# Kernel tuning notes

Measured on AMD Instinct MI355X. Metric: run time of the kernel, lower is better.

The kernel has to match this reference:

```python
import math
import jax, jax.numpy as jnp
import numpy as np

D_MODEL, D_K, D_V = 512, 64, 64
B, S = 4, 4096

def setup_inputs() -> dict:
    key = jax.random.key(0)
    ks = jax.random.split(key, 7)
    scale_in = 1.0 / math.sqrt(D_MODEL)
    return {
        "x": jax.random.normal(ks[0], (B, S, D_MODEL), dtype=jnp.float32),
        "wq": jax.random.normal(ks[1], (D_MODEL, D_K), dtype=jnp.float32) * scale_in,
        "bq": jax.random.normal(ks[2], (D_K,), dtype=jnp.float32) * 0.02,
        "wk": jax.random.normal(ks[3], (D_MODEL, D_K), dtype=jnp.float32) * scale_in,
        "bk": jax.random.normal(ks[4], (D_K,), dtype=jnp.float32) * 0.02,
        "wv": jax.random.normal(ks[5], (D_MODEL, D_V), dtype=jnp.float32) * scale_in,
        "bv": jax.random.normal(ks[6], (D_V,), dtype=jnp.float32) * 0.02,
    }

def reference(x, wq, bq, wk, bk, wv, bv):
    # q,k: [B,S,Dk]; v: [B,S,Dv]
    q = jnp.einsum("bsd,dk->bsk", x, wq) + bq
    k = jnp.einsum("bsd,dk->bsk", x, wk) + bk
    v = jnp.einsum("bsd,dv->bsv", x, wv) + bv
    inv_sqrt_dk = 1.0 / math.sqrt(D_K)
    scores = jnp.einsum("bqk,bsk->bqs", q, k) * inv_sqrt_dk  # [B,S,S]
    probs = jax.nn.softmax(scores, axis=2)
    return jnp.einsum("bqs,bsv->bqv", probs, v)  # [B,S,Dv]
```

## Files before the change

kernel.cpp:

```cpp
#include <hip/hip_runtime.h>
#include <hip/hip_bf16.h>
#include <cstddef>
#include <cstdint>

#define DM 512
#define DK 64
#define BB 4
#define S4 4096
#define NR (BB*S4)
#define KVB 64
#define QBLOCK 128
#define LP 72

typedef float   f32x16 __attribute__((ext_vector_type(16)));
typedef short   bf16x8 __attribute__((ext_vector_type(8)));

#define QSCALE 0.18033688011112042f

__device__ __forceinline__ ushort bf16bits(float f) {
    __hip_bfloat16 h = __float2bfloat16(f);
    return *reinterpret_cast<ushort*>(&h);
}

__device__ __forceinline__ uint32_t cvtpk(float a, float b) {
    uint32_t d;
    asm("v_cvt_pk_bf16_f32 %0, %1, %2" : "=v"(d) : "v"(a), "v"(b));
    return d;
}

__device__ __forceinline__ void permswap(uint32_t& a, uint32_t& b) {
    asm("v_permlane32_swap_b32 %0, %1" : "+v"(a), "+v"(b));
}

__global__ __launch_bounds__(256) void prep_w(
    const float* __restrict__ wq, const float* __restrict__ wk,
    const float* __restrict__ wv,
    ushort* __restrict__ Wfh, ushort* __restrict__ Wfl)
{
    const int id = blockIdx.x * 256 + threadIdx.x;
    const int c  = id >> 9, k = id & 511;
    const float* src = (c < 64) ? wq : (c < 128) ? wk : wv;
    const float wval = src[k * DK + (c & 63)];
    const ushort h  = bf16bits(wval);
    __hip_bfloat16 hh = *reinterpret_cast<const __hip_bfloat16*>(&h);
    const ushort l  = bf16bits(wval - __bfloat162float(hh));
    const int ko = k >> 6, ks = (k >> 4) & 3, kh = (k >> 3) & 1, e = k & 7;
    const size_t idx = ((size_t)((ko * 4 + ks) * 2 + kh) * 192 + c) * 8 + e;
    Wfh[idx] = h;
    Wfl[idx] = l;
}

__global__ __launch_bounds__(256, 3) void qkv_mfma(
    const float* __restrict__ x,
    const ushort* __restrict__ Wfh, const ushort* __restrict__ Wfl,
    const float* __restrict__ bq, const float* __restrict__ bk,
    const float* __restrict__ bv,
    ushort* __restrict__ Qb, ushort* __restrict__ Kb, ushort* __restrict__ Vt)
{
    __shared__ ushort Xw[4][2][32 * 72];

    const int tid  = threadIdx.x;
    const int w    = tid >> 6;
    const int lane = tid & 63;
    const int hi   = lane >> 5;
    const int q5   = lane & 31;
    const int wr   = w >> 1, wc = w & 1;
    const size_t row0 = (size_t)blockIdx.x * 64;
    const int cidx = blockIdx.y * 2 + wc;
    const int lrow = lane >> 4;
    const int lcol = lane & 15;

    float4 xr[8];
    uint2  cw[8];

    auto gx = [&](int ko) {
        #pragma unroll
        for (int i = 0; i < 8; ++i) {
            const int r = wr * 32 + i * 4 + lrow;
            xr[i] = *(const float4*)&x[(row0 + r) * DM + ko * 64 + lcol * 4];
        }
    };
    auto cvt_all = [&]() {
        #pragma unroll
        for (int i = 0; i < 8; ++i)
            cw[i] = (uint2){cvtpk(xr[i].x, xr[i].y), cvtpk(xr[i].z, xr[i].w)};
    };
    auto wstage = [&](int buf) {
        ushort* base = &Xw[w][buf][0];
        #pragma unroll
        for (int i = 0; i < 8; ++i) {
            const int r = i * 4 + lrow;
            *reinterpret_cast<uint2*>(&base[r * 72 + lcol * 4]) = cw[i];
        }
    };

    f32x16 acc = {};

    gx(0); cvt_all(); wstage(0);
    gx(1);

    for (int ko = 0; ko < 8; ++ko) {
        const int cur = ko & 1;
        if (ko < 7) { cvt_all(); wstage(cur ^ 1); }
        if (ko < 6) gx(ko + 2);

        const ushort* Xc = &Xw[w][cur][0];
        #pragma unroll
        for (int ks = 0; ks < 4; ++ks) {
            const bf16x8 ah = *reinterpret_cast<const bf16x8*>(
                &Xc[q5 * 72 + ks * 16 + hi * 8]);
            const int seg = (ko * 4 + ks) * 2 + hi;
            const size_t wb = ((size_t)seg * 192 + cidx * 32 + q5) * 8;
            const bf16x8 bh = *reinterpret_cast<const bf16x8*>(Wfh + wb);
            const bf16x8 bl = *reinterpret_cast<const bf16x8*>(Wfl + wb);
            acc = __builtin_amdgcn_mfma_f32_32x32x16_bf16(ah, bh, acc, 0, 0, 0);
            acc = __builtin_amdgcn_mfma_f32_32x32x16_bf16(ah, bl, acc, 0, 0, 0);
        }
    }

    const int mi = cidx >> 1, half = cidx & 1;
    const float* bp[3] = {bq, bk, bv};
    const float bias = bp[mi][half * 32 + q5];

    if (blockIdx.y == 2) {
        __syncthreads();
        ushort* vt = &Xw[0][0][0];
        #pragma unroll
        for (int r = 0; r < 16; ++r) {
            const int rr = (r & 3) + 8 * (r >> 2) + 4 * hi;
            vt[(half * 32 + q5) * 72 + wr * 32 + rr] = bf16bits(acc[r] + bias);
        }
        __syncthreads();
        const int dv = tid >> 2, sc = tid & 3;
        const int bb = (int)(row0 >> 12);
        const int sb = (int)(row0 & (S4 - 1));
        const ushort* src = vt + dv * 72 + sc * 16;
        uint4* dst = reinterpret_cast<uint4*>(
            Vt + ((size_t)bb * DK + dv) * S4 + sb + sc * 16);
        dst[0] = *reinterpret_cast<const uint4*>(src);
        dst[1] = *reinterpret_cast<const uint4*>(src + 8);
    } else {
        ushort* op = (mi == 0) ? Qb : Kb;
        #pragma unroll
        for (int r = 0; r < 16; ++r) {
            const int rr = (r & 3) + 8 * (r >> 2) + 4 * hi;
            const size_t grow = row0 + wr * 32 + rr;
            float v = acc[r] + bias;
            if (mi == 0) v *= QSCALE;
            op[grow * DK + half * 32 + q5] = bf16bits(v);
        }
    }
}

__global__ __launch_bounds__(256, 4) void attn_mfma(
    const ushort* __restrict__ Qb, const ushort* __restrict__ Kb,
    const ushort* __restrict__ Vt,
    float* __restrict__ Opart, float* __restrict__ Lpart,
    float* __restrict__ out, int sigma)
{
    __shared__ ushort Ks[2][64 * LP];
    __shared__ ushort Vs[2][64 * LP];

    const int tid  = threadIdx.x;
    const int w    = tid >> 6;
    const int lane = tid & 63;
    const int hi   = lane >> 5;
    const int q5   = lane & 31;
    const int b    = blockIdx.y, ci = blockIdx.z;
    const int klen = S4 / sigma, kv0 = ci * klen;
    const int qrow = blockIdx.x * QBLOCK + w * 32 + q5;

    const int c0 = tid, c1 = tid + 256;
    const int r0 = c0 >> 3, cc0 = c0 & 7;
    const int r1 = c1 >> 3, cc1 = c1 & 7;

    bf16x8 qf[4];
    {
        const ushort* qp = Qb + ((size_t)b * S4 + qrow) * DK;
        #pragma unroll
        for (int s = 0; s < 4; ++s)
            qf[s] = *reinterpret_cast<const bf16x8*>(qp + s * 16 + hi * 8);
    }

    bf16x8 onesv;
    #pragma unroll
    for (int i = 0; i < 8; ++i) onesv[i] = (short)0x3F80;

    f32x16 oacc0 = {}, oacc1 = {}, lacc = {};

    uint4 kreg0, kreg1, vreg0, vreg1;
    auto gload = [&](int t) {
        const ushort* gK = Kb + ((size_t)b * S4 + kv0 + t * KVB) * DK;
        const ushort* gV = Vt + (size_t)b * DK * S4 + (kv0 + t * KVB);
        kreg0 = *reinterpret_cast<const uint4*>(gK + r0 * DK + cc0 * 8);
        kreg1 = *reinterpret_cast<const uint4*>(gK + r1 * DK + cc1 * 8);
        vreg0 = *reinterpret_cast<const uint4*>(gV + (size_t)r0 * S4 + cc0 * 8);
        vreg1 = *reinterpret_cast<const uint4*>(gV + (size_t)r1 * S4 + cc1 * 8);
    };
    auto stage = [&](int buf) {
        *reinterpret_cast<uint4*>(&Ks[buf][r0 * LP + cc0 * 8]) = kreg0;
        *reinterpret_cast<uint4*>(&Ks[buf][r1 * LP + cc1 * 8]) = kreg1;
        *reinterpret_cast<uint4*>(&Vs[buf][r0 * LP + cc0 * 8]) = vreg0;
        *reinterpret_cast<uint4*>(&Vs[buf][r1 * LP + cc1 * 8]) = vreg1;
    };

    const int nt = klen / KVB;
    gload(0);
    stage(0);
    if (nt > 1) gload(1);
    __syncthreads();

    for (int t = 0; t < nt; ++t) {
        const int cur = t & 1;
        if (t + 1 < nt) {
            stage(cur ^ 1);
            if (t + 2 < nt) gload(t + 2);
        }
        const ushort* Kbuf = &Ks[cur][0];
        const ushort* Vbuf = &Vs[cur][0];

        #pragma unroll
        for (int sub = 0; sub < 2; ++sub) {
            const int kvr = sub * 32 + q5;
            bf16x8 kf[4];
            #pragma unroll
            for (int s = 0; s < 4; ++s)
                kf[s] = *reinterpret_cast<const bf16x8*>(
                    &Kbuf[kvr * LP + (2 * s + hi) * 8]);
            f32x16 sacc = {};
            #pragma unroll
            for (int s = 0; s < 4; ++s)
                sacc = __builtin_amdgcn_mfma_f32_32x32x16_bf16(
                    kf[s], qf[s], sacc, 0, 0, 0);

            float p[16];
            #pragma unroll
            for (int r = 0; r < 16; ++r) p[r] = exp2f(sacc[r]);

            uint32_t wd[8];
            #pragma unroll
            for (int g = 0; g < 4; ++g) {
                wd[2 * g]     = cvtpk(p[4 * g],     p[4 * g + 1]);
                wd[2 * g + 1] = cvtpk(p[4 * g + 2], p[4 * g + 3]);
            }
            permswap(wd[0], wd[2]);  permswap(wd[1], wd[3]);
            permswap(wd[4], wd[6]);  permswap(wd[5], wd[7]);
            union { uint32_t u[4]; bf16x8 v; } pa0, pa1;
            pa0.u[0] = wd[0]; pa0.u[1] = wd[1]; pa0.u[2] = wd[2]; pa0.u[3] = wd[3];
            pa1.u[0] = wd[4]; pa1.u[1] = wd[5]; pa1.u[2] = wd[6]; pa1.u[3] = wd[7];

            lacc = __builtin_amdgcn_mfma_f32_32x32x16_bf16(pa0.v, onesv, lacc, 0, 0, 0);
            lacc = __builtin_amdgcn_mfma_f32_32x32x16_bf16(pa1.v, onesv, lacc, 0, 0, 0);

            #pragma unroll
            for (int h = 0; h < 2; ++h) {
                const int dv = h * 32 + q5;
                #pragma unroll
                for (int tt = 0; tt < 2; ++tt) {
                    const bf16x8 vf = *reinterpret_cast<const bf16x8*>(
                        &Vbuf[dv * LP + (sub * 4 + tt * 2 + hi) * 8]);
                    if (h == 0)
                        oacc0 = __builtin_amdgcn_mfma_f32_32x32x16_bf16(
                            tt == 0 ? pa0.v : pa1.v, vf, oacc0, 0, 0, 0);
                    else
                        oacc1 = __builtin_amdgcn_mfma_f32_32x32x16_bf16(
                            tt == 0 ? pa0.v : pa1.v, vf, oacc1, 0, 0, 0);
                }
            }
        }
        __syncthreads();
    }

    if (sigma == 1) {
        #pragma unroll
        for (int r = 0; r < 16; ++r) {
            const int qq = (r & 3) + 8 * (r >> 2) + 4 * hi;
            const float inv = 1.0f / lacc[r];
            const size_t row = (size_t)b * S4 + blockIdx.x * QBLOCK + w * 32 + qq;
            out[row * DK + q5]      = oacc0[r] * inv;
            out[row * DK + 32 + q5] = oacc1[r] * inv;
        }
    } else {
        if (q5 == 0) {
            #pragma unroll
            for (int r = 0; r < 16; ++r) {
                const int qq = (r & 3) + 8 * (r >> 2) + 4 * hi;
                const size_t row = (size_t)b * S4 + blockIdx.x * QBLOCK + w * 32 + qq;
                Lpart[(size_t)ci * NR + row] = lacc[r];
            }
        }
        #pragma unroll
        for (int r = 0; r < 16; ++r) {
            const int qq = (r & 3) + 8 * (r >> 2) + 4 * hi;
            const size_t row = (size_t)b * S4 + blockIdx.x * QBLOCK + w * 32 + qq;
            float* op = Opart + ((size_t)ci * NR + row) * DK;
            op[q5]      = oacc0[r];
            op[32 + q5] = oacc1[r];
        }
    }
}

__global__ __launch_bounds__(256) void attn_reduce(
    const float* __restrict__ Opart, const float* __restrict__ Lpart,
    float* __restrict__ out, int sigma)
{
    const int e4  = blockIdx.x * 256 + threadIdx.x;
    const int row = e4 >> 4;
    const int d4  = e4 & 15;

    float L = 0.0f;
    float4 O = {0.0f, 0.0f, 0.0f, 0.0f};
    for (int i = 0; i < sigma; ++i) {
        L += Lpart[(size_t)i * NR + row];
        const float4 o = *reinterpret_cast<const float4*>(
            Opart + (((size_t)i * NR + row) << 6) + d4 * 4);
        O.x += o.x; O.y += o.y; O.z += o.z; O.w += o.w;
    }
    const float inv = 1.0f / L;
    float4 res = {O.x * inv, O.y * inv, O.z * inv, O.w * inv};
    *reinterpret_cast<float4*>(out + ((size_t)row << 6) + d4 * 4) = res;
}

extern "C" void kernel_launch(void* const* d_in, const int* in_sizes, int n_in,
                              void* d_out, int out_size, void* d_ws, size_t ws_size,
                              hipStream_t stream)
{
    const float* x  = (const float*)d_in[0];
    const float* wq = (const float*)d_in[1];
    const float* bq = (const float*)d_in[2];
    const float* wk = (const float*)d_in[3];
    const float* bk = (const float*)d_in[4];
    const float* wv = (const float*)d_in[5];
    const float* bv = (const float*)d_in[6];

    char* ws = (char*)d_ws;
    const size_t MB2  = (size_t)NR * DK * 2;
    const size_t WTSZ = (size_t)192 * DM * 2;

    ushort* Qb  = (ushort*)(ws);
    ushort* Kb  = (ushort*)(ws + MB2);
    ushort* Vt  = (ushort*)(ws + 2 * MB2);
    ushort* Wfh = (ushort*)(ws + 3 * MB2);
    ushort* Wfl = (ushort*)(ws + 3 * MB2 + WTSZ);

    const size_t POFF = 3 * MB2 + 2 * WTSZ;

    int sigma = 1;
    const int cand[2] = {4, 2};
    for (int i = 0; i < 2; ++i) {
        const int s = cand[i];
        const size_t need = POFF + (size_t)s * ((size_t)NR * DK * 4 + (size_t)NR * 4);
        if (need <= ws_size) { sigma = s; break; }
    }

    float* Opart = (float*)(ws + POFF);
    float* Lpart = (float*)(ws + POFF + (size_t)sigma * NR * DK * 4);

    prep_w<<<384, 256, 0, stream>>>(wq, wk, wv, Wfh, Wfl);
    qkv_mfma<<<dim3(NR / 64, 3), 256, 0, stream>>>(x, Wfh, Wfl, bq, bk, bv,
                                                   Qb, Kb, Vt);

    dim3 grid(S4 / QBLOCK, BB, sigma);
    attn_mfma<<<grid, 256, 0, stream>>>(Qb, Kb, Vt, Opart, Lpart,
                                        (float*)d_out, sigma);

    if (sigma > 1)
        attn_reduce<<<(NR * DK) / 1024, 256, 0, stream>>>(Opart, Lpart,
                                                          (float*)d_out, sigma);
}
```

Measured before the change: 64.46 us.

## Split KV across warps within block and reduce partials in shared memory

Each block now handles 32 query rows, and its four warps each take a quarter of the key/value sequence through private double-buffered LDS tiles, so the per-tile block-wide barriers go away. The partial outputs and row sums are combined in shared memory at the end, which replaces the global Opart/Lpart split-K buffers and the separate reduce kernel launch. In exchange each block uses far more LDS (about 72 KB), occupancy drops to 2 blocks per CU, and every warp reloads the same Q fragment while streaming its own K/V with no reuse across warps.

```diff
diff --git a/kernel.cpp b/kernel.cpp
--- a/kernel.cpp
+++ b/kernel.cpp
@@ -8,9 +8,9 @@
 #define BB 4
 #define S4 4096
 #define NR (BB*S4)
-#define KVB 64
-#define QBLOCK 128
-#define LP 72
+#define QW 32
+#define KTILE 2304
+#define VTILE 2304
 
 typedef float   f32x16 __attribute__((ext_vector_type(16)));
 typedef short   bf16x8 __attribute__((ext_vector_type(8)));
@@ -152,27 +152,28 @@
     }
 }
 
-__global__ __launch_bounds__(256, 4) void attn_mfma(
+__global__ __launch_bounds__(256, 2) void attn_mfma(
     const ushort* __restrict__ Qb, const ushort* __restrict__ Kb,
-    const ushort* __restrict__ Vt,
-    float* __restrict__ Opart, float* __restrict__ Lpart,
-    float* __restrict__ out, int sigma)
+    const ushort* __restrict__ Vt, float* __restrict__ out)
 {
-    __shared__ ushort Ks[2][64 * LP];
-    __shared__ ushort Vs[2][64 * LP];
+    __shared__ ushort KV[4][2][KTILE + VTILE];
 
     const int tid  = threadIdx.x;
     const int w    = tid >> 6;
     const int lane = tid & 63;
     const int hi   = lane >> 5;
     const int q5   = lane & 31;
-    const int b    = blockIdx.y, ci = blockIdx.z;
-    const int klen = S4 / sigma, kv0 = ci * klen;
-    const int qrow = blockIdx.x * QBLOCK + w * 32 + q5;
-
-    const int c0 = tid, c1 = tid + 256;
-    const int r0 = c0 >> 3, cc0 = c0 & 7;
-    const int r1 = c1 >> 3, cc1 = c1 & 7;
+    const int b    = blockIdx.y;
+    const int kvw  = w * (S4 / 4);
+    const int qrow = blockIdx.x * QW + q5;
+
+    int kr[4], kc[4], dv[4], vc[4];
+    #pragma unroll
+    for (int i = 0; i < 4; ++i) {
+        const int c = i * 64 + lane;
+        kr[i] = c >> 3;  kc[i] = c & 7;
+        dv[i] = c >> 2;  vc[i] = c & 3;
+    }
 
     bf16x8 qf[4];
     {
@@ -188,27 +189,29 @@
 
     f32x16 oacc0 = {}, oacc1 = {}, lacc = {};
 
-    uint4 kreg0, kreg1, vreg0, vreg1;
+    uint4 kreg[4], vreg[4];
     auto gload = [&](int t) {
-        const ushort* gK = Kb + ((size_t)b * S4 + kv0 + t * KVB) * DK;
-        const ushort* gV = Vt + (size_t)b * DK * S4 + (kv0 + t * KVB);
-        kreg0 = *reinterpret_cast<const uint4*>(gK + r0 * DK + cc0 * 8);
-        kreg1 = *reinterpret_cast<const uint4*>(gK + r1 * DK + cc1 * 8);
-        vreg0 = *reinterpret_cast<const uint4*>(gV + (size_t)r0 * S4 + cc0 * 8);
-        vreg1 = *reinterpret_cast<const uint4*>(gV + (size_t)r1 * S4 + cc1 * 8);
+        const ushort* gK = Kb + ((size_t)b * S4 + kvw + t * 32) * DK;
+        const ushort* gV = Vt + (size_t)b * DK * S4 + (kvw + t * 32);
+        #pragma unroll
+        for (int i = 0; i < 4; ++i) {
+            kreg[i] = *reinterpret_cast<const uint4*>(gK + kr[i] * DK + kc[i] * 8);
+            vreg[i] = *reinterpret_cast<const uint4*>(gV + (size_t)dv[i] * S4 + vc[i] * 8);
+        }
     };
     auto stage = [&](int buf) {
-        *reinterpret_cast<uint4*>(&Ks[buf][r0 * LP + cc0 * 8]) = kreg0;
-        *reinterpret_cast<uint4*>(&Ks[buf][r1 * LP + cc1 * 8]) = kreg1;
-        *reinterpret_cast<uint4*>(&Vs[buf][r0 * LP + cc0 * 8]) = vreg0;
-        *reinterpret_cast<uint4*>(&Vs[buf][r1 * LP + cc1 * 8]) = vreg1;
-    };
-
-    const int nt = klen / KVB;
-    gload(0);
-    stage(0);
-    if (nt > 1) gload(1);
-    __syncthreads();
+        ushort* Kl = &KV[w][buf][0];
+        ushort* Vl = &KV[w][buf][KTILE];
+        #pragma unroll
+        for (int i = 0; i < 4; ++i) {
+            *reinterpret_cast<uint4*>(&Kl[kr[i] * 72 + kc[i] * 8]) = kreg[i];
+            *reinterpret_cast<uint4*>(&Vl[dv[i] * 36 + vc[i] * 8]) = vreg[i];
+        }
+    };
+
+    const int nt = (S4 / 4) / 32;
+    gload(0); stage(0);
+    gload(1);
 
     for (int t = 0; t < nt; ++t) {
         const int cur = t & 1;
@@ -216,109 +219,76 @@
             stage(cur ^ 1);
             if (t + 2 < nt) gload(t + 2);
         }
-        const ushort* Kbuf = &Ks[cur][0];
-        const ushort* Vbuf = &Vs[cur][0];
-
-        #pragma unroll
-        for (int sub = 0; sub < 2; ++sub) {
-            const int kvr = sub * 32 + q5;
-            bf16x8 kf[4];
+        const ushort* Kbuf = &KV[w][cur][0];
+        const ushort* Vbuf = &KV[w][cur][KTILE];
+
+        bf16x8 kf[4];
+        #pragma unroll
+        for (int s = 0; s < 4; ++s)
+            kf[s] = *reinterpret_cast<const bf16x8*>(
+                &Kbuf[q5 * 72 + (2 * s + hi) * 8]);
+        f32x16 sacc = {};
+        #pragma unroll
+        for (int s = 0; s < 4; ++s)
+            sacc = __builtin_amdgcn_mfma_f32_32x32x16_bf16(
+                kf[s], qf[s], sacc, 0, 0, 0);
+
+        float p[16];
+        #pragma unroll
+        for (int r = 0; r < 16; ++r) p[r] = exp2f(sacc[r]);
+
+        uint32_t wd[8];
+        #pragma unroll
+        for (int g = 0; g < 4; ++g) {
+            wd[2 * g]     = cvtpk(p[4 * g],     p[4 * g + 1]);
+            wd[2 * g + 1] = cvtpk(p[4 * g + 2], p[4 * g + 3]);
+        }
+        permswap(wd[0], wd[2]);  permswap(wd[1], wd[3]);
+        permswap(wd[4], wd[6]);  permswap(wd[5], wd[7]);
+        union { uint32_t u[4]; bf16x8 v; } pa0, pa1;
+        pa0.u[0] = wd[0]; pa0.u[1] = wd[1]; pa0.u[2] = wd[2]; pa0.u[3] = wd[3];
+        pa1.u[0] = wd[4]; pa1.u[1] = wd[5]; pa1.u[2] = wd[6]; pa1.u[3] = wd[7];
+
+        lacc = __builtin_amdgcn_mfma_f32_32x32x16_bf16(pa0.v, onesv, lacc, 0, 0, 0);
+        lacc = __builtin_amdgcn_mfma_f32_32x32x16_bf16(pa1.v, onesv, lacc, 0, 0, 0);
+
+        #pragma unroll
+        for (int h = 0; h < 2; ++h) {
+            const int dvr = h * 32 + q5;
             #pragma unroll
-            for (int s = 0; s < 4; ++s)
-                kf[s] = *reinterpret_cast<const bf16x8*>(
-                    &Kbuf[kvr * LP + (2 * s + hi) * 8]);
-            f32x16 sacc = {};
-            #pragma unroll
-            for (int s = 0; s < 4; ++s)
-                sacc = __builtin_amdgcn_mfma_f32_32x32x16_bf16(
-                    kf[s], qf[s], sacc, 0, 0, 0);
-
-            float p[16];
-            #pragma unroll
-            for (int r = 0; r < 16; ++r) p[r] = exp2f(sacc[r]);
-
-            uint32_t wd[8];
-            #pragma unroll
-            for (int g = 0; g < 4; ++g) {
-                wd[2 * g]     = cvtpk(p[4 * g],     p[4 * g + 1]);
-                wd[2 * g + 1] = cvtpk(p[4 * g + 2], p[4 * g + 3]);
+            for (int tt = 0; tt < 2; ++tt) {
+                const bf16x8 vf = *reinterpret_cast<const bf16x8*>(
+                    &Vbuf[dvr * 36 + (tt * 2 + hi) * 8]);
+                if (h == 0)
+                    oacc0 = __builtin_amdgcn_mfma_f32_32x32x16_bf16(
+                        tt == 0 ? pa0.v : pa1.v, vf, oacc0, 0, 0, 0);
+                else
+                    oacc1 = __builtin_amdgcn_mfma_f32_32x32x16_bf16(
+                        tt == 0 ? pa0.v : pa1.v, vf, oacc1, 0, 0, 0);
             }
-            permswap(wd[0], wd[2]);  permswap(wd[1], wd[3]);
-            permswap(wd[4], wd[6]);  permswap(wd[5], wd[7]);
-            union { uint32_t u[4]; bf16x8 v; } pa0, pa1;
-            pa0.u[0] = wd[0]; pa0.u[1] = wd[1]; pa0.u[2] = wd[2]; pa0.u[3] = wd[3];
-            pa1.u[0] = wd[4]; pa1.u[1] = wd[5]; pa1.u[2] = wd[6]; pa1.u[3] = wd[7];
-
-            lacc = __builtin_amdgcn_mfma_f32_32x32x16_bf16(pa0.v, onesv, lacc, 0, 0, 0);
-            lacc = __builtin_amdgcn_mfma_f32_32x32x16_bf16(pa1.v, onesv, lacc, 0, 0, 0);
-
-            #pragma unroll
-            for (int h = 0; h < 2; ++h) {
-                const int dv = h * 32 + q5;
-                #pragma unroll
-                for (int tt = 0; tt < 2; ++tt) {
-                    const bf16x8 vf = *reinterpret_cast<const bf16x8*>(
-                        &Vbuf[dv * LP + (sub * 4 + tt * 2 + hi) * 8]);
-                    if (h == 0)
-                        oacc0 = __builtin_amdgcn_mfma_f32_32x32x16_bf16(
-                            tt == 0 ? pa0.v : pa1.v, vf, oacc0, 0, 0, 0);
-                    else
-                        oacc1 = __builtin_amdgcn_mfma_f32_32x32x16_bf16(
-                            tt == 0 ? pa0.v : pa1.v, vf, oacc1, 0, 0, 0);
-                }
-            }
-        }
-        __syncthreads();
-    }
-
-    if (sigma == 1) {
-        #pragma unroll
-        for (int r = 0; r < 16; ++r) {
-            const int qq = (r & 3) + 8 * (r >> 2) + 4 * hi;
-            const float inv = 1.0f / lacc[r];
-            const size_t row = (size_t)b * S4 + blockIdx.x * QBLOCK + w * 32 + qq;
-            out[row * DK + q5]      = oacc0[r] * inv;
-            out[row * DK + 32 + q5] = oacc1[r] * inv;
-        }
-    } else {
-        if (q5 == 0) {
-            #pragma unroll
-            for (int r = 0; r < 16; ++r) {
-                const int qq = (r & 3) + 8 * (r >> 2) + 4 * hi;
-                const size_t row = (size_t)b * S4 + blockIdx.x * QBLOCK + w * 32 + qq;
-                Lpart[(size_t)ci * NR + row] = lacc[r];
-            }
-        }
-        #pragma unroll
-        for (int r = 0; r < 16; ++r) {
-            const int qq = (r & 3) + 8 * (r >> 2) + 4 * hi;
-            const size_t row = (size_t)b * S4 + blockIdx.x * QBLOCK + w * 32 + qq;
-            float* op = Opart + ((size_t)ci * NR + row) * DK;
-            op[q5]      = oacc0[r];
-            op[32 + q5] = oacc1[r];
-        }
-    }
-}
-
-__global__ __launch_bounds__(256) void attn_reduce(
-    const float* __restrict__ Opart, const float* __restrict__ Lpart,
-    float* __restrict__ out, int sigma)
-{
-    const int e4  = blockIdx.x * 256 + threadIdx.x;
-    const int row = e4 >> 4;
-    const int d4  = e4 & 15;
-
-    float L = 0.0f;
-    float4 O = {0.0f, 0.0f, 0.0f, 0.0f};
-    for (int i = 0; i < sigma; ++i) {
-        L += Lpart[(size_t)i * NR + row];
-        const float4 o = *reinterpret_cast<const float4*>(
-            Opart + (((size_t)i * NR + row) << 6) + d4 * 4);
-        O.x += o.x; O.y += o.y; O.z += o.z; O.w += o.w;
-    }
-    const float inv = 1.0f / L;
-    float4 res = {O.x * inv, O.y * inv, O.z * inv, O.w * inv};
-    *reinterpret_cast<float4*>(out + ((size_t)row << 6) + d4 * 4) = res;
+        }
+    }
+
+    __syncthreads();
+    float* Ob = reinterpret_cast<float*>(&KV[0][0][0]);
+    float* Lb = Ob + 4 * 2048;
+    #pragma unroll
+    for (int r = 0; r < 16; ++r) {
+        const int qq = (r & 3) + 8 * (r >> 2) + 4 * hi;
+        Ob[w * 2048 + qq * 64 + q5]      = oacc0[r];
+        Ob[w * 2048 + qq * 64 + 32 + q5] = oacc1[r];
+        if (q5 == 0) Lb[w * 32 + qq] = lacc[r];
+    }
+    __syncthreads();
+    #pragma unroll
+    for (int i = 0; i < 8; ++i) {
+        const int e   = i * 256 + tid;
+        const int row = e >> 6, d = e & 63;
+        const float Osum = Ob[row * 64 + d] + Ob[2048 + row * 64 + d]
+                         + Ob[4096 + row * 64 + d] + Ob[6144 + row * 64 + d];
+        const float Lsum = Lb[row] + Lb[32 + row] + Lb[64 + row] + Lb[96 + row];
+        out[((size_t)b * S4 + blockIdx.x * QW + row) * DK + d] = Osum / Lsum;
+    }
 }
 
 extern "C" void kernel_launch(void* const* d_in, const int* in_sizes, int n_in,
@@ -343,28 +313,10 @@
     ushort* Wfh = (ushort*)(ws + 3 * MB2);
     ushort* Wfl = (ushort*)(ws + 3 * MB2 + WTSZ);
 
-    const size_t POFF = 3 * MB2 + 2 * WTSZ;
-
-    int sigma = 1;
-    const int cand[2] = {4, 2};
-    for (int i = 0; i < 2; ++i) {
-        const int s = cand[i];
-        const size_t need = POFF + (size_t)s * ((size_t)NR * DK * 4 + (size_t)NR * 4);
-        if (need <= ws_size) { sigma = s; break; }
-    }
-
-    float* Opart = (float*)(ws + POFF);
-    float* Lpart = (float*)(ws + POFF + (size_t)sigma * NR * DK * 4);
-
     prep_w<<<384, 256, 0, stream>>>(wq, wk, wv, Wfh, Wfl);
     qkv_mfma<<<dim3(NR / 64, 3), 256, 0, stream>>>(x, Wfh, Wfl, bq, bk, bv,
                                                    Qb, Kb, Vt);
 
-    dim3 grid(S4 / QBLOCK, BB, sigma);
-    attn_mfma<<<grid, 256, 0, stream>>>(Qb, Kb, Vt, Opart, Lpart,
-                                        (float*)d_out, sigma);
-
-    if (sigma > 1)
-        attn_reduce<<<(NR * DK) / 1024, 256, 0, stream>>>(Opart, Lpart,
-                                                          (float*)d_out, sigma);
-}
+    dim3 grid(S4 / QW, BB);
+    attn_mfma<<<grid, 256, 0, stream>>>(Qb, Kb, Vt, (float*)d_out);
+}
```

After: 164.2 us. 2.55x slower.
